# Kernel optimization log

Measured on AMD Instinct MI355X. Metric: run time of the kernel, lower is better.

## Reference

```python
import jax, jax.numpy as jnp
import numpy as np

B, L, D, H = 2, 2048, 1024, 16
HD = D // H  # head_dim = 64


def setup_inputs() -> dict:
    key = jax.random.key(0)
    ks = jax.random.split(key, 9)
    s = 0.02
    return {
        "x": jax.random.normal(ks[0], (B, L, D), dtype=jnp.float32),
        "wq": jax.random.normal(ks[1], (D, D), dtype=jnp.float32) * s,
        "bq": jnp.zeros((D,), dtype=jnp.float32),
        "wk": jax.random.normal(ks[2], (D, D), dtype=jnp.float32) * s,
        "bk": jnp.zeros((D,), dtype=jnp.float32),
        "wv": jax.random.normal(ks[3], (D, D), dtype=jnp.float32) * s,
        "bv": jnp.zeros((D,), dtype=jnp.float32),
        "wo": jax.random.normal(ks[4], (D, D), dtype=jnp.float32) * s,
        "bo": jnp.zeros((D,), dtype=jnp.float32),
    }


def reference(x, wq, bq, wk, bk, wv, bv, wo, bo):
    b, l, d = x.shape
    # projections -> [B, H, L, HD]
    def split_heads(t):
        return t.reshape(b, l, H, HD).transpose(0, 2, 1, 3)
    q = split_heads(x @ wq + bq)
    k = split_heads(x @ wk + bk)
    v = split_heads(x @ wv + bv)
    scores = jnp.einsum('bhqd,bhkd->bhqk', q, k) / jnp.sqrt(jnp.float32(HD))
    # causal mask via -inf then clamp to [-50, 50]: masked entries become -50 (faithful to torch code)
    mask = jnp.triu(jnp.full((l, l), -jnp.inf, dtype=scores.dtype), k=1)
    scores = jnp.clip(scores + mask[None, None, :, :], -50.0, 50.0)
    attn = jax.nn.softmax(scores, axis=-1)
    # dropout is identity in eval/deterministic mode
    out = jnp.einsum('bhqk,bhkd->bhqd', attn, v)
    out = out.transpose(0, 2, 1, 3).reshape(b, l, d)
    out = out @ wo + bo
    return out, attn
```

## Files before the change

### kernel.cpp

```cpp
#include <hip/hip_runtime.h>
#include <hip/hip_bf16.h>

#define B_  2
#define L_  2048
#define D_  1024
#define H_  16
#define HD_ 64

typedef __bf16 bf16x8 __attribute__((ext_vector_type(8)));
typedef float  f32x4  __attribute__((ext_vector_type(4)));
using bf16_t = __hip_bfloat16;
typedef unsigned int u32;
typedef unsigned long long u64;

static __device__ __forceinline__ f32x4 mfma16(bf16x8 a, bf16x8 b, f32x4 c) {
    return __builtin_amdgcn_mfma_f32_16x16x32_bf16(a, b, c, 0, 0, 0);
}

static __device__ __forceinline__ void gl16(const bf16_t* g, bf16_t* l) {
    __builtin_amdgcn_global_load_lds(
        (const __attribute__((address_space(1))) unsigned int*)g,
        (__attribute__((address_space(3))) unsigned int*)l, 16, 0, 0);
}

static __device__ __forceinline__ u32 cvtpk(float lo, float hi) {
    u32 r;
    asm("v_cvt_pk_bf16_f32 %0, %1, %2" : "=v"(r) : "v"(lo), "v"(hi));
    return r;
}

__global__ __launch_bounds__(256) void k_prep(
        const float* __restrict__ x,
        const float* __restrict__ w0, const float* __restrict__ w1,
        const float* __restrict__ w2, const float* __restrict__ w3,
        bf16_t* __restrict__ xb,
        bf16_t* __restrict__ t0, bf16_t* __restrict__ t1,
        bf16_t* __restrict__ t2, bf16_t* __restrict__ t3) {
    __shared__ bf16_t tile[64][65];
    int z = blockIdx.z;
    int t = threadIdx.x;
    if (z >= 4) {
        int slice = z - 4;
        int lin = blockIdx.y * 16 + blockIdx.x;
        int idx = (slice * 256 + lin) * 256 + t;
        const float4* p = (const float4*)x + (size_t)idx * 2;
        float4 a = p[0], b = p[1];
        union { bf16_t h[8]; bf16x8 v; } u;
        u.h[0] = __float2bfloat16(a.x); u.h[1] = __float2bfloat16(a.y);
        u.h[2] = __float2bfloat16(a.z); u.h[3] = __float2bfloat16(a.w);
        u.h[4] = __float2bfloat16(b.x); u.h[5] = __float2bfloat16(b.y);
        u.h[6] = __float2bfloat16(b.z); u.h[7] = __float2bfloat16(b.w);
        *(bf16x8*)(xb + (size_t)idx * 8) = u.v;
        return;
    }
    const float* w = (z == 0) ? w0 : (z == 1) ? w1 : (z == 2) ? w2 : w3;
    bf16_t* wt     = (z == 0) ? t0 : (z == 1) ? t1 : (z == 2) ? t2 : t3;
    int kb = blockIdx.x * 64, nb = blockIdx.y * 64;
    int r  = t >> 4, c4 = (t & 15) * 4;
    #pragma unroll
    for (int it = 0; it < 4; ++it) {
        int kr = r + it * 16;
        float4 v = *(const float4*)&w[(size_t)(kb + kr) * D_ + nb + c4];
        tile[kr][c4 + 0] = __float2bfloat16(v.x);
        tile[kr][c4 + 1] = __float2bfloat16(v.y);
        tile[kr][c4 + 2] = __float2bfloat16(v.z);
        tile[kr][c4 + 3] = __float2bfloat16(v.w);
    }
    __syncthreads();
    #pragma unroll
    for (int it = 0; it < 4; ++it) {
        int nr = r + it * 16;
        union { bf16_t h[4]; u64 u; } o;
        o.h[0] = tile[c4 + 0][nr];
        o.h[1] = tile[c4 + 1][nr];
        o.h[2] = tile[c4 + 2][nr];
        o.h[3] = tile[c4 + 3][nr];
        *(u64*)&wt[(size_t)(nb + nr) * D_ + kb + c4] = o.u;
    }
}

__global__ __launch_bounds__(256, 3) void k_gemm_qkv(
        const bf16_t* __restrict__ A,
        const bf16_t* __restrict__ Wq, const bf16_t* __restrict__ Wk, const bf16_t* __restrict__ Wv,
        const float* __restrict__ bq, const float* __restrict__ bk, const float* __restrict__ bv,
        bf16_t* __restrict__ Qo, bf16_t* __restrict__ Ko, bf16_t* __restrict__ Vo) {
    __shared__ __align__(16) bf16_t Al[128][32];
    __shared__ __align__(16) bf16_t Bl[128][32];
    const int K = D_;
    int z = blockIdx.z;
    const bf16_t* Wt = (z == 0) ? Wq : (z == 1) ? Wk : Wv;
    const float* bias = (z == 0) ? bq : (z == 1) ? bk : bv;
    bf16_t* outp      = (z == 0) ? Qo : (z == 1) ? Ko : Vo;
    int tid = threadIdx.x, lane = tid & 63, wid = tid >> 6;
    int m0 = blockIdx.y * 128, n0 = blockIdx.x * 128;
    int wm = (wid >> 1) * 64, wn = (wid & 1) * 64;
    int r16 = lane & 15, g = lane >> 4;
    int lrow = lane >> 2, lcol = (lane & 3) * 8;
    f32x4 acc[4][4] = {};
    for (int kb = 0; kb < K; kb += 32) {
        __syncthreads();
        gl16(&A [(size_t)(m0 + wid * 32 + lrow) * K + kb + lcol],      &Al[wid * 32][0]);
        gl16(&A [(size_t)(m0 + wid * 32 + 16 + lrow) * K + kb + lcol], &Al[wid * 32 + 16][0]);
        gl16(&Wt[(size_t)(n0 + wid * 32 + lrow) * K + kb + lcol],      &Bl[wid * 32][0]);
        gl16(&Wt[(size_t)(n0 + wid * 32 + 16 + lrow) * K + kb + lcol], &Bl[wid * 32 + 16][0]);
        __syncthreads();
        bf16x8 af[4], bfr[4];
        #pragma unroll
        for (int i = 0; i < 4; ++i) af[i]  = *(const bf16x8*)&Al[wm + i * 16 + r16][g * 8];
        #pragma unroll
        for (int j = 0; j < 4; ++j) bfr[j] = *(const bf16x8*)&Bl[wn + j * 16 + r16][g * 8];
        #pragma unroll
        for (int i = 0; i < 4; ++i)
            #pragma unroll
            for (int j = 0; j < 4; ++j)
                acc[i][j] = mfma16(af[i], bfr[j], acc[i][j]);
    }
    if (z == 2) {
        #pragma unroll
        for (int i = 0; i < 4; ++i)
            #pragma unroll
            for (int j = 0; j < 4; ++j) {
                int n = n0 + wn + j * 16 + r16;
                float bv2 = bias[n];
                int h = n >> 6, hd = n & 63;
                int m = m0 + wm + i * 16 + g * 4;
                int bb = m >> 11, l0 = m & (L_ - 1);
                u32 lo = cvtpk(acc[i][j][0] + bv2, acc[i][j][1] + bv2);
                u32 hi = cvtpk(acc[i][j][2] + bv2, acc[i][j][3] + bv2);
                u64 pk = ((u64)hi << 32) | lo;
                *(u64*)&Vo[(((size_t)(bb * H_ + h)) * HD_ + hd) * L_ + l0] = pk;
            }
    } else {
        #pragma unroll
        for (int i = 0; i < 4; ++i) {
            #pragma unroll
            for (int j = 0; j < 4; ++j) {
                int n = n0 + wn + j * 16 + r16;
                float bv2 = bias[n];
                int h = n >> 6, hd = n & 63;
                #pragma unroll
                for (int e = 0; e < 4; ++e) {
                    int m = m0 + wm + i * 16 + g * 4 + e;
                    float v = acc[i][j][e] + bv2;
                    int bb = m >> 11, l = m & (L_ - 1);
                    outp[(((size_t)(bb * H_ + h)) * L_ + l) * HD_ + hd] = __float2bfloat16(v);
                }
            }
        }
    }
}

__global__ __launch_bounds__(256, 2) void k_gemm_o(const bf16_t* __restrict__ A,
                                                   const bf16_t* __restrict__ Wt,
                                                   const float* __restrict__ bias,
                                                   float* __restrict__ outp) {
    __shared__ __align__(16) bf16_t Al[128][32];
    __shared__ __align__(16) bf16_t Bl[64][32];
    const int K = D_;
    int tid = threadIdx.x, lane = tid & 63, wid = tid >> 6;
    int m0 = blockIdx.y * 128, n0 = blockIdx.x * 64;
    int wm = (wid >> 1) * 64, wn = (wid & 1) * 32;
    int r16 = lane & 15, g = lane >> 4;
    int lrow = lane >> 2, lcol = (lane & 3) * 8;
    f32x4 acc[4][2] = {};
    for (int kb = 0; kb < K; kb += 32) {
        __syncthreads();
        gl16(&A [(size_t)(m0 + wid * 32 + lrow) * K + kb + lcol],      &Al[wid * 32][0]);
        gl16(&A [(size_t)(m0 + wid * 32 + 16 + lrow) * K + kb + lcol], &Al[wid * 32 + 16][0]);
        gl16(&Wt[(size_t)(n0 + wid * 16 + lrow) * K + kb + lcol],      &Bl[wid * 16][0]);
        __syncthreads();
        bf16x8 af[4], bfr[2];
        #pragma unroll
        for (int i = 0; i < 4; ++i) af[i]  = *(const bf16x8*)&Al[wm + i * 16 + r16][g * 8];
        #pragma unroll
        for (int j = 0; j < 2; ++j) bfr[j] = *(const bf16x8*)&Bl[wn + j * 16 + r16][g * 8];
        #pragma unroll
        for (int i = 0; i < 4; ++i)
            #pragma unroll
            for (int j = 0; j < 2; ++j)
                acc[i][j] = mfma16(af[i], bfr[j], acc[i][j]);
    }
    #pragma unroll
    for (int i = 0; i < 4; ++i)
        #pragma unroll
        for (int j = 0; j < 2; ++j) {
            int n = n0 + wn + j * 16 + r16;
            float bv = bias[n];
            #pragma unroll
            for (int e = 0; e < 4; ++e) {
                int m = m0 + wm + i * 16 + g * 4 + e;
                outp[(size_t)m * D_ + n] = acc[i][j][e] + bv;
            }
        }
}

__global__ __launch_bounds__(256, 4) void k_attn(const bf16_t* __restrict__ Q,
                                                 const bf16_t* __restrict__ Kb,
                                                 const bf16_t* __restrict__ VT,
                                                 bf16_t* __restrict__ ctx,
                                                 float* __restrict__ attn) {
    __shared__ __align__(16) bf16_t K_lds[2][64][64];
    __shared__ __align__(16) bf16_t V_lds[2][64][64];
    int tid = threadIdx.x, lane = tid & 63, wid = tid >> 6;
    int bid = blockIdx.x;
    int idx = bid >> 3;
    int bh  = (bid & 7) + 8 * (idx & 3);
    int qt  = 31 - (idx >> 2);
    int b = bh >> 4, h = bh & 15;
    int qb = qt * 64;
    const int diag = qt;
    const bf16_t* Qh = Q  + (size_t)bh * L_ * HD_;
    const bf16_t* Kh = Kb + (size_t)bh * L_ * HD_;
    const bf16_t* Vh = VT + (size_t)bh * HD_ * L_;
    int r16 = lane & 15, g = lane >> 4;
    const float scale2 = 0.125f * 1.44269504088896340736f;
    const float clamp2 = 50.0f * 1.44269504088896340736f;
    int qrow0 = qb + wid * 16;
    int qrow  = qrow0 + r16;

    {
        int zs = qb + 64;
        f32x4 z4 = {0.f, 0.f, 0.f, 0.f};
        for (int r = 0; r < 16; ++r) {
            float* rowp = attn + ((size_t)bh * L_ + qrow0 + r) * L_;
            for (int c = zs + lane * 4; c < L_; c += 256)
                __builtin_nontemporal_store(z4, (f32x4*)&rowp[c]);
        }
    }

    bf16x8 q0 = *(const bf16x8*)&Qh[(size_t)(qrow0 + r16) * HD_ + g * 8];
    bf16x8 q1 = *(const bf16x8*)&Qh[(size_t)(qrow0 + r16) * HD_ + 32 + g * 8];

    int srow = lane >> 3, sunit = ((lane & 7) ^ (lane >> 3)) * 8;
    auto STAGE_K = [&](int kt1, int nxt) {
        #pragma unroll
        for (int i = 0; i < 2; ++i) {
            int cb = wid * 16 + i * 8;
            gl16(&Kh[(size_t)(kt1 * 64 + cb + srow) * HD_ + sunit], &K_lds[nxt][cb][0]);
        }
    };
    auto STAGE_V = [&](int kt1, int nxt) {
        #pragma unroll
        for (int i = 0; i < 2; ++i) {
            int cb = wid * 16 + i * 8;
            gl16(&Vh[(size_t)(cb + srow) * L_ + kt1 * 64 + sunit], &V_lds[nxt][cb][0]);
        }
    };

    f32x4 ctxa[4] = {};
    float zsum = 0.f;
    int rx = r16 & 7;

    STAGE_K(0, 0); STAGE_V(0, 0);
    int cur = 0;
    for (int kt = 0; kt <= diag; ++kt) {
        __syncthreads();
        int nxt = cur ^ 1;
        if (kt < diag) { STAGE_K(kt + 1, nxt); STAGE_V(kt + 1, nxt); }
        int kb = kt * 64;
        #pragma unroll
        for (int sub = 0; sub < 2; ++sub) {
            f32x4 sa[2];
            #pragma unroll
            for (int sp = 0; sp < 2; ++sp) {
                int krow = sub * 32 + sp * 16 + r16;
                bf16x8 kf0 = *(const bf16x8*)&K_lds[cur][krow][(g ^ rx) * 8];
                bf16x8 kf1 = *(const bf16x8*)&K_lds[cur][krow][((4 + g) ^ rx) * 8];
                f32x4 zz = {};
                sa[sp] = mfma16(kf1, q1, mfma16(kf0, q0, zz));
            }
            int kb2 = kb + sub * 32;
            u32 dw[2][2];
            #pragma unroll
            for (int sp = 0; sp < 2; ++sp) {
                float ev[4];
                #pragma unroll
                for (int e = 0; e < 4; ++e) {
                    int key = kb2 + sp * 16 + g * 4 + e;
                    float sc = fminf(fmaxf(sa[sp][e] * scale2, -clamp2), clamp2);
                    ev[e] = (key > qrow) ? 0.f : exp2f(sc);
                    zsum += ev[e];
                }
                dw[sp][0] = cvtpk(ev[0], ev[1]);
                dw[sp][1] = cvtpk(ev[2], ev[3]);
            }
            union { u32 u[4]; bf16x8 v; } pa;
            pa.u[0] = dw[0][0]; pa.u[1] = dw[0][1];
            pa.u[2] = dw[1][0]; pa.u[3] = dw[1][1];
            #pragma unroll
            for (int t = 0; t < 4; ++t) {
                int vrow = t * 16 + r16;
                int u0 = ((sub * 4 + (g >> 1)) ^ rx) * 8 + (g & 1) * 4;
                int u1 = ((sub * 4 + 2 + (g >> 1)) ^ rx) * 8 + (g & 1) * 4;
                union { u64 d[2]; bf16x8 v; } vf;
                vf.d[0] = *(const u64*)&V_lds[cur][vrow][u0];
                vf.d[1] = *(const u64*)&V_lds[cur][vrow][u1];
                ctxa[t] = mfma16(pa.v, vf.v, ctxa[t]);
            }
        }
        cur = nxt;
    }

    __syncthreads();
    STAGE_K(0, 0);

    float v = zsum;
    v += __shfl_xor(v, 16);
    v += __shfl_xor(v, 32);
    float invz = 1.f / v;

    #pragma unroll
    for (int e = 0; e < 4; ++e) {
        float izq = __shfl(invz, g * 4 + e);
        int qr = qrow0 + g * 4 + e;
        #pragma unroll
        for (int t = 0; t < 4; ++t)
            ctx[((size_t)b * L_ + qr) * D_ + h * HD_ + t * 16 + r16] =
                __float2bfloat16(ctxa[t][e] * izq);
    }

    cur = 0;
    for (int kt = 0; kt <= diag; ++kt) {
        __syncthreads();
        int nxt = cur ^ 1;
        if (kt < diag) STAGE_K(kt + 1, nxt);
        int kb = kt * 64;
        #pragma unroll
        for (int sub = 0; sub < 2; ++sub)
            #pragma unroll
            for (int sp = 0; sp < 2; ++sp) {
                int krow = sub * 32 + sp * 16 + r16;
                bf16x8 kf0 = *(const bf16x8*)&K_lds[cur][krow][(g ^ rx) * 8];
                bf16x8 kf1 = *(const bf16x8*)&K_lds[cur][krow][((4 + g) ^ rx) * 8];
                f32x4 zz = {};
                f32x4 sa = mfma16(kf1, q1, mfma16(kf0, q0, zz));
                int cb = kb + sub * 32 + sp * 16 + g * 4;
                f32x4 fv;
                #pragma unroll
                for (int e = 0; e < 4; ++e) {
                    int key = cb + e;
                    float sc = fminf(fmaxf(sa[e] * scale2, -clamp2), clamp2);
                    fv[e] = (key > qrow) ? 0.f : exp2f(sc) * invz;
                }
                __builtin_nontemporal_store(fv,
                    (f32x4*)&attn[((size_t)bh * L_ + qrow) * L_ + cb]);
            }
        cur = nxt;
    }
}

extern "C" void kernel_launch(void* const* d_in, const int* in_sizes, int n_in,
                              void* d_out, int out_size, void* d_ws, size_t ws_size,
                              hipStream_t stream) {
    const float* x  = (const float*)d_in[0];
    const float* wq = (const float*)d_in[1];
    const float* bq = (const float*)d_in[2];
    const float* wk = (const float*)d_in[3];
    const float* bk = (const float*)d_in[4];
    const float* wv = (const float*)d_in[5];
    const float* bv = (const float*)d_in[6];
    const float* wo = (const float*)d_in[7];
    const float* bo = (const float*)d_in[8];

    char* ws = (char*)d_ws;
    bf16_t* xb   = (bf16_t*)(ws);
    bf16_t* wqt  = (bf16_t*)(ws + ( 8u << 20));
    bf16_t* wkt  = (bf16_t*)(ws + (10u << 20));
    bf16_t* wvt  = (bf16_t*)(ws + (12u << 20));
    bf16_t* wot  = (bf16_t*)(ws + (14u << 20));
    bf16_t* Qb   = (bf16_t*)(ws + (16u << 20));
    bf16_t* Kbuf = (bf16_t*)(ws + (24u << 20));
    bf16_t* VTb  = (bf16_t*)(ws + (32u << 20));
    bf16_t* ctxb = (bf16_t*)(ws + (40u << 20));

    float* out  = (float*)d_out;
    float* attn = out + (size_t)B_ * L_ * D_;

    dim3 gp(16, 16, 12);
    k_prep<<<gp, 256, 0, stream>>>(x, wq, wk, wv, wo, xb, wqt, wkt, wvt, wot);

    dim3 g3(D_ / 128, (B_ * L_) / 128, 3);
    k_gemm_qkv<<<g3, 256, 0, stream>>>(xb, wqt, wkt, wvt, bq, bk, bv, Qb, Kbuf, VTb);

    k_attn<<<1024, 256, 0, stream>>>(Qb, Kbuf, VTb, ctxb, attn);

    dim3 gg(D_ / 64, (B_ * L_) / 128);
    k_gemm_o<<<gg, 256, 0, stream>>>(ctxb, wot, bo, (float*)d_out);
}
```

Baseline: 264.2 us.

## Split attention into PV pass and fused attn-write plus output-projection kernel

The fused attention kernel is split in two. The first kernel computes the context and the per-row inverse normaliser and writes the normaliser to a workspace buffer. The second kernel runs the output projection GEMM blocks alongside the blocks that recompute the probabilities and write the attention matrix, so the write-bound attention output overlaps with the GEMM. LDS staging of K and V is dropped in favour of direct global loads, which relies on cache hits and may raise load latency.

```diff
diff --git a/kernel.cpp b/kernel.cpp
--- a/kernel.cpp
+++ b/kernel.cpp
@@ -150,57 +150,11 @@
     }
 }
 
-__global__ __launch_bounds__(256, 2) void k_gemm_o(const bf16_t* __restrict__ A,
-                                                   const bf16_t* __restrict__ Wt,
-                                                   const float* __restrict__ bias,
-                                                   float* __restrict__ outp) {
-    __shared__ __align__(16) bf16_t Al[128][32];
-    __shared__ __align__(16) bf16_t Bl[64][32];
-    const int K = D_;
-    int tid = threadIdx.x, lane = tid & 63, wid = tid >> 6;
-    int m0 = blockIdx.y * 128, n0 = blockIdx.x * 64;
-    int wm = (wid >> 1) * 64, wn = (wid & 1) * 32;
-    int r16 = lane & 15, g = lane >> 4;
-    int lrow = lane >> 2, lcol = (lane & 3) * 8;
-    f32x4 acc[4][2] = {};
-    for (int kb = 0; kb < K; kb += 32) {
-        __syncthreads();
-        gl16(&A [(size_t)(m0 + wid * 32 + lrow) * K + kb + lcol],      &Al[wid * 32][0]);
-        gl16(&A [(size_t)(m0 + wid * 32 + 16 + lrow) * K + kb + lcol], &Al[wid * 32 + 16][0]);
-        gl16(&Wt[(size_t)(n0 + wid * 16 + lrow) * K + kb + lcol],      &Bl[wid * 16][0]);
-        __syncthreads();
-        bf16x8 af[4], bfr[2];
-        #pragma unroll
-        for (int i = 0; i < 4; ++i) af[i]  = *(const bf16x8*)&Al[wm + i * 16 + r16][g * 8];
-        #pragma unroll
-        for (int j = 0; j < 2; ++j) bfr[j] = *(const bf16x8*)&Bl[wn + j * 16 + r16][g * 8];
-        #pragma unroll
-        for (int i = 0; i < 4; ++i)
-            #pragma unroll
-            for (int j = 0; j < 2; ++j)
-                acc[i][j] = mfma16(af[i], bfr[j], acc[i][j]);
-    }
-    #pragma unroll
-    for (int i = 0; i < 4; ++i)
-        #pragma unroll
-        for (int j = 0; j < 2; ++j) {
-            int n = n0 + wn + j * 16 + r16;
-            float bv = bias[n];
-            #pragma unroll
-            for (int e = 0; e < 4; ++e) {
-                int m = m0 + wm + i * 16 + g * 4 + e;
-                outp[(size_t)m * D_ + n] = acc[i][j][e] + bv;
-            }
-        }
-}
-
-__global__ __launch_bounds__(256, 4) void k_attn(const bf16_t* __restrict__ Q,
-                                                 const bf16_t* __restrict__ Kb,
-                                                 const bf16_t* __restrict__ VT,
-                                                 bf16_t* __restrict__ ctx,
-                                                 float* __restrict__ attn) {
-    __shared__ __align__(16) bf16_t K_lds[2][64][64];
-    __shared__ __align__(16) bf16_t V_lds[2][64][64];
+__global__ __launch_bounds__(256, 4) void k_pv(const bf16_t* __restrict__ Q,
+                                               const bf16_t* __restrict__ Kb,
+                                               const bf16_t* __restrict__ VT,
+                                               bf16_t* __restrict__ ctx,
+                                               float* __restrict__ invzbuf) {
     int tid = threadIdx.x, lane = tid & 63, wid = tid >> 6;
     int bid = blockIdx.x;
     int idx = bid >> 3;
@@ -218,6 +172,132 @@
     int qrow0 = qb + wid * 16;
     int qrow  = qrow0 + r16;
 
+    bf16x8 q0 = *(const bf16x8*)&Qh[(size_t)qrow * HD_ + g * 8];
+    bf16x8 q1 = *(const bf16x8*)&Qh[(size_t)qrow * HD_ + 32 + g * 8];
+
+    f32x4 ctxa[4] = {};
+    float zsum = 0.f;
+
+    for (int kt = 0; kt <= diag; ++kt) {
+        #pragma unroll
+        for (int sub = 0; sub < 2; ++sub) {
+            int krow0 = kt * 64 + sub * 32;
+            f32x4 sa[2];
+            #pragma unroll
+            for (int sp = 0; sp < 2; ++sp) {
+                const bf16_t* kp = &Kh[(size_t)(krow0 + sp * 16 + r16) * HD_ + g * 8];
+                bf16x8 kf0 = *(const bf16x8*)kp;
+                bf16x8 kf1 = *(const bf16x8*)(kp + 32);
+                f32x4 zz = {};
+                sa[sp] = mfma16(kf1, q1, mfma16(kf0, q0, zz));
+            }
+            u32 dw[2][2];
+            #pragma unroll
+            for (int sp = 0; sp < 2; ++sp) {
+                float ev[4];
+                #pragma unroll
+                for (int e = 0; e < 4; ++e) {
+                    int key = krow0 + sp * 16 + g * 4 + e;
+                    float sc = fminf(fmaxf(sa[sp][e] * scale2, -clamp2), clamp2);
+                    ev[e] = (key > qrow) ? 0.f : exp2f(sc);
+                    zsum += ev[e];
+                }
+                dw[sp][0] = cvtpk(ev[0], ev[1]);
+                dw[sp][1] = cvtpk(ev[2], ev[3]);
+            }
+            union { u32 u[4]; bf16x8 v; } pa;
+            pa.u[0] = dw[0][0]; pa.u[1] = dw[0][1];
+            pa.u[2] = dw[1][0]; pa.u[3] = dw[1][1];
+            #pragma unroll
+            for (int t = 0; t < 4; ++t) {
+                const bf16_t* vp = &Vh[(size_t)(t * 16 + r16) * L_ + krow0 + g * 4];
+                union { u64 d[2]; bf16x8 v; } vf;
+                vf.d[0] = *(const u64*)vp;
+                vf.d[1] = *(const u64*)(vp + 16);
+                ctxa[t] = mfma16(pa.v, vf.v, ctxa[t]);
+            }
+        }
+    }
+
+    float v = zsum;
+    v += __shfl_xor(v, 16);
+    v += __shfl_xor(v, 32);
+    float invz = 1.f / v;
+    if (g == 0) invzbuf[(size_t)bh * L_ + qrow] = invz;
+
+    #pragma unroll
+    for (int e = 0; e < 4; ++e) {
+        float izq = __shfl(invz, g * 4 + e);
+        int qr = qrow0 + g * 4 + e;
+        #pragma unroll
+        for (int t = 0; t < 4; ++t)
+            ctx[((size_t)b * L_ + qr) * D_ + h * HD_ + t * 16 + r16] =
+                __float2bfloat16(ctxa[t][e] * izq);
+    }
+}
+
+__global__ __launch_bounds__(256, 4) void k_wr_o(
+        const bf16_t* __restrict__ Q, const bf16_t* __restrict__ Kb,
+        const float* __restrict__ invzbuf, float* __restrict__ attn,
+        const bf16_t* __restrict__ ctxb, const bf16_t* __restrict__ Wo,
+        const float* __restrict__ bo, float* __restrict__ outp) {
+    __shared__ __align__(16) bf16_t Al[128][32];
+    __shared__ __align__(16) bf16_t Bl[64][32];
+    int tid = threadIdx.x, lane = tid & 63, wid = tid >> 6;
+    int bid = blockIdx.x;
+    int r16 = lane & 15, g = lane >> 4;
+
+    if (bid < 512) {
+        const int K = D_;
+        int m0 = (bid >> 4) * 128, n0 = (bid & 15) * 64;
+        int wm = (wid >> 1) * 64, wn = (wid & 1) * 32;
+        int lrow = lane >> 2, lcol = (lane & 3) * 8;
+        f32x4 acc[4][2] = {};
+        for (int kb = 0; kb < K; kb += 32) {
+            __syncthreads();
+            gl16(&ctxb[(size_t)(m0 + wid * 32 + lrow) * K + kb + lcol],      &Al[wid * 32][0]);
+            gl16(&ctxb[(size_t)(m0 + wid * 32 + 16 + lrow) * K + kb + lcol], &Al[wid * 32 + 16][0]);
+            gl16(&Wo  [(size_t)(n0 + wid * 16 + lrow) * K + kb + lcol],      &Bl[wid * 16][0]);
+            __syncthreads();
+            bf16x8 af[4], bfr[2];
+            #pragma unroll
+            for (int i = 0; i < 4; ++i) af[i]  = *(const bf16x8*)&Al[wm + i * 16 + r16][g * 8];
+            #pragma unroll
+            for (int j = 0; j < 2; ++j) bfr[j] = *(const bf16x8*)&Bl[wn + j * 16 + r16][g * 8];
+            #pragma unroll
+            for (int i = 0; i < 4; ++i)
+                #pragma unroll
+                for (int j = 0; j < 2; ++j)
+                    acc[i][j] = mfma16(af[i], bfr[j], acc[i][j]);
+        }
+        #pragma unroll
+        for (int i = 0; i < 4; ++i)
+            #pragma unroll
+            for (int j = 0; j < 2; ++j) {
+                int n = n0 + wn + j * 16 + r16;
+                float bv = bo[n];
+                #pragma unroll
+                for (int e = 0; e < 4; ++e) {
+                    int m = m0 + wm + i * 16 + g * 4 + e;
+                    outp[(size_t)m * D_ + n] = acc[i][j][e] + bv;
+                }
+            }
+        return;
+    }
+
+    int wbid = bid - 512;
+    int idx = wbid >> 3;
+    int bh  = (wbid & 7) + 8 * (idx & 3);
+    int qt  = 31 - (idx >> 2);
+    int qb = qt * 64;
+    const int diag = qt;
+    const bf16_t* Qh = Q  + (size_t)bh * L_ * HD_;
+    const bf16_t* Kh = Kb + (size_t)bh * L_ * HD_;
+    const float scale2 = 0.125f * 1.44269504088896340736f;
+    const float clamp2 = 50.0f * 1.44269504088896340736f;
+    int qrow0 = qb + wid * 16;
+    int qrow  = qrow0 + r16;
+
     {
         int zs = qb + 64;
         f32x4 z4 = {0.f, 0.f, 0.f, 0.f};
@@ -228,113 +308,22 @@
         }
     }
 
-    bf16x8 q0 = *(const bf16x8*)&Qh[(size_t)(qrow0 + r16) * HD_ + g * 8];
-    bf16x8 q1 = *(const bf16x8*)&Qh[(size_t)(qrow0 + r16) * HD_ + 32 + g * 8];
-
-    int srow = lane >> 3, sunit = ((lane & 7) ^ (lane >> 3)) * 8;
-    auto STAGE_K = [&](int kt1, int nxt) {
-        #pragma unroll
-        for (int i = 0; i < 2; ++i) {
-            int cb = wid * 16 + i * 8;
-            gl16(&Kh[(size_t)(kt1 * 64 + cb + srow) * HD_ + sunit], &K_lds[nxt][cb][0]);
-        }
-    };
-    auto STAGE_V = [&](int kt1, int nxt) {
-        #pragma unroll
-        for (int i = 0; i < 2; ++i) {
-            int cb = wid * 16 + i * 8;
-            gl16(&Vh[(size_t)(cb + srow) * L_ + kt1 * 64 + sunit], &V_lds[nxt][cb][0]);
-        }
-    };
-
-    f32x4 ctxa[4] = {};
-    float zsum = 0.f;
-    int rx = r16 & 7;
-
-    STAGE_K(0, 0); STAGE_V(0, 0);
-    int cur = 0;
+    float invz = invzbuf[(size_t)bh * L_ + qrow];
+    bf16x8 q0 = *(const bf16x8*)&Qh[(size_t)qrow * HD_ + g * 8];
+    bf16x8 q1 = *(const bf16x8*)&Qh[(size_t)qrow * HD_ + 32 + g * 8];
+
     for (int kt = 0; kt <= diag; ++kt) {
-        __syncthreads();
-        int nxt = cur ^ 1;
-        if (kt < diag) { STAGE_K(kt + 1, nxt); STAGE_V(kt + 1, nxt); }
-        int kb = kt * 64;
         #pragma unroll
         for (int sub = 0; sub < 2; ++sub) {
-            f32x4 sa[2];
+            int krow0 = kt * 64 + sub * 32;
             #pragma unroll
             for (int sp = 0; sp < 2; ++sp) {
-                int krow = sub * 32 + sp * 16 + r16;
-                bf16x8 kf0 = *(const bf16x8*)&K_lds[cur][krow][(g ^ rx) * 8];
-                bf16x8 kf1 = *(const bf16x8*)&K_lds[cur][krow][((4 + g) ^ rx) * 8];
-                f32x4 zz = {};
-                sa[sp] = mfma16(kf1, q1, mfma16(kf0, q0, zz));
-            }
-            int kb2 = kb + sub * 32;
-            u32 dw[2][2];
-            #pragma unroll
-            for (int sp = 0; sp < 2; ++sp) {
-                float ev[4];
-                #pragma unroll
-                for (int e = 0; e < 4; ++e) {
-                    int key = kb2 + sp * 16 + g * 4 + e;
-                    float sc = fminf(fmaxf(sa[sp][e] * scale2, -clamp2), clamp2);
-                    ev[e] = (key > qrow) ? 0.f : exp2f(sc);
-                    zsum += ev[e];
-                }
-                dw[sp][0] = cvtpk(ev[0], ev[1]);
-                dw[sp][1] = cvtpk(ev[2], ev[3]);
-            }
-            union { u32 u[4]; bf16x8 v; } pa;
-            pa.u[0] = dw[0][0]; pa.u[1] = dw[0][1];
-            pa.u[2] = dw[1][0]; pa.u[3] = dw[1][1];
-            #pragma unroll
-            for (int t = 0; t < 4; ++t) {
-                int vrow = t * 16 + r16;
-                int u0 = ((sub * 4 + (g >> 1)) ^ rx) * 8 + (g & 1) * 4;
-                int u1 = ((sub * 4 + 2 + (g >> 1)) ^ rx) * 8 + (g & 1) * 4;
-                union { u64 d[2]; bf16x8 v; } vf;
-                vf.d[0] = *(const u64*)&V_lds[cur][vrow][u0];
-                vf.d[1] = *(const u64*)&V_lds[cur][vrow][u1];
-                ctxa[t] = mfma16(pa.v, vf.v, ctxa[t]);
-            }
-        }
-        cur = nxt;
-    }
-
-    __syncthreads();
-    STAGE_K(0, 0);
-
-    float v = zsum;
-    v += __shfl_xor(v, 16);
-    v += __shfl_xor(v, 32);
-    float invz = 1.f / v;
-
-    #pragma unroll
-    for (int e = 0; e < 4; ++e) {
-        float izq = __shfl(invz, g * 4 + e);
-        int qr = qrow0 + g * 4 + e;
-        #pragma unroll
-        for (int t = 0; t < 4; ++t)
-            ctx[((size_t)b * L_ + qr) * D_ + h * HD_ + t * 16 + r16] =
-                __float2bfloat16(ctxa[t][e] * izq);
-    }
-
-    cur = 0;
-    for (int kt = 0; kt <= diag; ++kt) {
-        __syncthreads();
-        int nxt = cur ^ 1;
-        if (kt < diag) STAGE_K(kt + 1, nxt);
-        int kb = kt * 64;
-        #pragma unroll
-        for (int sub = 0; sub < 2; ++sub)
-            #pragma unroll
-            for (int sp = 0; sp < 2; ++sp) {
-                int krow = sub * 32 + sp * 16 + r16;
-                bf16x8 kf0 = *(const bf16x8*)&K_lds[cur][krow][(g ^ rx) * 8];
-                bf16x8 kf1 = *(const bf16x8*)&K_lds[cur][krow][((4 + g) ^ rx) * 8];
+                const bf16_t* kp = &Kh[(size_t)(krow0 + sp * 16 + r16) * HD_ + g * 8];
+                bf16x8 kf0 = *(const bf16x8*)kp;
+                bf16x8 kf1 = *(const bf16x8*)(kp + 32);
                 f32x4 zz = {};
                 f32x4 sa = mfma16(kf1, q1, mfma16(kf0, q0, zz));
-                int cb = kb + sub * 32 + sp * 16 + g * 4;
+                int cb = krow0 + sp * 16 + g * 4;
                 f32x4 fv;
                 #pragma unroll
                 for (int e = 0; e < 4; ++e) {
@@ -345,7 +334,7 @@
                 __builtin_nontemporal_store(fv,
                     (f32x4*)&attn[((size_t)bh * L_ + qrow) * L_ + cb]);
             }
-        cur = nxt;
+        }
     }
 }
 
@@ -372,6 +361,7 @@
     bf16_t* Kbuf = (bf16_t*)(ws + (24u << 20));
     bf16_t* VTb  = (bf16_t*)(ws + (32u << 20));
     bf16_t* ctxb = (bf16_t*)(ws + (40u << 20));
+    float*  invzbuf = (float*)(ws + (52u << 20));
 
     float* out  = (float*)d_out;
     float* attn = out + (size_t)B_ * L_ * D_;
@@ -382,8 +372,7 @@
     dim3 g3(D_ / 128, (B_ * L_) / 128, 3);
     k_gemm_qkv<<<g3, 256, 0, stream>>>(xb, wqt, wkt, wvt, bq, bk, bv, Qb, Kbuf, VTb);
 
-    k_attn<<<1024, 256, 0, stream>>>(Qb, Kbuf, VTb, ctxb, attn);
-
-    dim3 gg(D_ / 64, (B_ * L_) / 128);
-    k_gemm_o<<<gg, 256, 0, stream>>>(ctxb, wot, bo, (float*)d_out);
-}
+    k_pv<<<1024, 256, 0, stream>>>(Qb, Kbuf, VTb, ctxb, invzbuf);
+
+    k_wr_o<<<1536, 256, 0, stream>>>(Qb, Kbuf, invzbuf, attn, ctxb, wot, bo, (float*)d_out);
+}
```

Measured after the change: 434.6 us. 1.64x slower.
